# Optimization experiments

Measured on AMD Instinct MI355X. Metric: run time of the kernel, lower is better.

Reference implementation:

```python
import jax, jax.numpy as jnp
import numpy as np

D_MODEL = 2048
N_HEADS = 16
N_KV = 4
GROUP = N_HEADS // N_KV  # 4
D_K = D_MODEL // N_HEADS  # 128
D_V = D_MODEL // N_KV     # 512
THETA = 10000.0
Q_DIM = N_HEADS * D_K
K_DIM = N_KV * D_K
V_DIM = N_KV * D_V


def _apply_rope(t, sin, cos):
    # t: [B, H, L, D]; sin/cos: [L, D] broadcast over batch/heads
    half = t.shape[-1] // 2
    x1, x2 = t[..., :half], t[..., half:]
    rot = jnp.concatenate([-x2, x1], axis=-1)
    return t * cos + rot * sin


def setup_inputs() -> dict:
    key = jax.random.key(0)
    k1, k2, k3 = jax.random.split(key, 3)
    x = jax.random.normal(k1, (2, 2048, D_MODEL), dtype=jnp.float32)
    # attn_proj: Linear(d_model -> Q_DIM+K_DIM+V_DIM, bias=False); stored as [in, out]
    W_attn = jax.random.normal(k2, (D_MODEL, Q_DIM + K_DIM + V_DIM), dtype=jnp.float32) * 0.02
    # out_proj: Linear(n_heads*d_v -> d_model) with bias
    W_out = jax.random.normal(k3, (N_HEADS * D_V, D_MODEL), dtype=jnp.float32) * 0.02
    b_out = jnp.zeros((D_MODEL,), dtype=jnp.float32)
    return {"x": x, "W_attn": W_attn, "W_out": W_out, "b_out": b_out}


def reference(x, W_attn, W_out, b_out):
    B, L, _ = x.shape
    qkv = x @ W_attn  # [B, L, Q_DIM+K_DIM+V_DIM]
    q = qkv[..., :Q_DIM].reshape(B, L, N_HEADS, D_K).transpose(0, 2, 1, 3)          # [B,H,L,dk]
    k = qkv[..., Q_DIM:Q_DIM + K_DIM].reshape(B, L, N_KV, D_K).transpose(0, 2, 1, 3)  # [B,Hkv,L,dk]
    v = qkv[..., Q_DIM + K_DIM:].reshape(B, L, N_KV, D_V).transpose(0, 2, 1, 3)       # [B,Hkv,L,dv]

    # RoPE (computed in float32, as in source)
    inv_freq = 1.0 / (THETA ** (jnp.arange(0, D_K, 2, dtype=jnp.float32) / D_K))
    freqs = jnp.arange(L, dtype=jnp.float32)[:, None] * inv_freq[None, :]  # [L, dk/2]
    ang = jnp.concatenate([freqs, freqs], axis=-1)                          # [L, dk]
    sin, cos = jnp.sin(ang), jnp.cos(ang)
    q = _apply_rope(q.astype(jnp.float32), sin, cos).astype(x.dtype)
    k = _apply_rope(k.astype(jnp.float32), sin, cos).astype(x.dtype)

    # GQA: repeat_interleave(group, dim=1) is equivalent to grouping q heads as [kv, group]
    qg = q.reshape(B, N_KV, GROUP, L, D_K)
    scores = jnp.einsum('bkgqd,bkld->bkgql', qg, k) / (D_K ** 0.5)  # [B,Hkv,G,L,L]
    probs = jax.nn.softmax(scores, axis=-1)
    ctx = jnp.einsum('bkgql,bkle->bkgqe', probs, v)  # [B,Hkv,G,L,dv]
    ctx = ctx.reshape(B, N_HEADS, L, D_V).transpose(0, 2, 1, 3).reshape(B, L, N_HEADS * D_V)
    return ctx @ W_out + b_out
```

## Files before the change

kernel.cpp:

```cpp
#include <hip/hip_runtime.h>

typedef unsigned short u16;
typedef float f32x4 __attribute__((ext_vector_type(4)));
typedef __bf16 bf16x8 __attribute__((ext_vector_type(8)));

#define DEV static __device__ __forceinline__

DEV u16 f2bf(float f) {
  union { float f; unsigned u; } c; c.f = f;
  unsigned u = c.u;
  u += 0x7fffu + ((u >> 16) & 1u);
  return (u16)(u >> 16);
}
DEV float bf2f(u16 h) {
  union { float f; unsigned u; } c; c.u = ((unsigned)h) << 16;
  return c.f;
}
DEV f32x4 MFMA(bf16x8 a, bf16x8 b, f32x4 c) {
  return __builtin_amdgcn_mfma_f32_16x16x32_bf16(a, b, c, 0, 0, 0);
}
DEV unsigned cvt_pk_bf16(float a, float b) {
  unsigned r;
  asm("v_cvt_pk_bf16_f32 %0, %1, %2" : "=v"(r) : "v"(a), "v"(b));
  return r;
}
DEV float ex2(float x) { return __builtin_amdgcn_exp2f(x); }
DEV void glds16(const void* src, void* lds) {
  __builtin_amdgcn_global_load_lds(
      (__attribute__((address_space(1))) void*)src,
      (__attribute__((address_space(3))) void*)lds, 16, 0, 0);
}
DEV void barrier_raw() {
  __builtin_amdgcn_sched_barrier(0);
  asm volatile("s_barrier" ::: "memory");
  __builtin_amdgcn_sched_barrier(0);
}
#define VMCNT(N)                                              \
  do {                                                        \
    asm volatile("s_waitcnt vmcnt(" #N ")" ::: "memory");     \
    __builtin_amdgcn_sched_barrier(0);                        \
  } while (0)


__global__ void prep_kernel(const float* __restrict__ x, const float* __restrict__ W_attn,
                            float* __restrict__ sinT, float* __restrict__ cosT,
                            u16* __restrict__ xb, u16* __restrict__ WbT) {
  __shared__ u16 tile[64][72];
  const int bk = blockIdx.x, t = threadIdx.x;
  if (bk < 512) {
    int idx = bk * 256 + t;
    int l = idx >> 6, i = idx & 63;
    float inv = __expf(-((float)(2 * i) / 128.0f) * 9.210340371976184f);
    float ang = (float)l * inv;
    sinT[idx] = sinf(ang);
    cosT[idx] = cosf(ang);
  } else if (bk < 8704) {
    int i = ((bk - 512) * 256 + t) * 4;
    float4 v = *(const float4*)(x + i);
    ushort4 o;
    o.x = f2bf(v.x); o.y = f2bf(v.y); o.z = f2bf(v.z); o.w = f2bf(v.w);
    *(ushort4*)(xb + i) = o;
  } else {
    int idx = bk - 8704;
    int c0 = (idx % 72) * 64, r0 = (idx / 72) * 64;
    int tc = (t & 15) * 4, tr = t >> 4;
#pragma unroll
    for (int i = 0; i < 4; ++i) {
      int r = tr + i * 16;
      float4 v = *(const float4*)(W_attn + (size_t)(r0 + r) * 4608 + c0 + tc);
      tile[tc + 0][r] = f2bf(v.x);
      tile[tc + 1][r] = f2bf(v.y);
      tile[tc + 2][r] = f2bf(v.z);
      tile[tc + 3][r] = f2bf(v.w);
    }
    __syncthreads();
#pragma unroll
    for (int i = 0; i < 4; ++i) {
      int cc = tr + i * 16;
      ushort4 o;
      o.x = tile[cc][tc]; o.y = tile[cc][tc + 1];
      o.z = tile[cc][tc + 2]; o.w = tile[cc][tc + 3];
      *(ushort4*)(WbT + (size_t)(c0 + cc) * 2048 + r0 + tc) = o;
    }
  }
}

__global__ void transpose_cast64(const float* __restrict__ in, u16* __restrict__ out,
                                 int R, int C) {
  __shared__ u16 tile[64][72];
  int c0 = blockIdx.x * 64, r0 = blockIdx.y * 64;
  int t = threadIdx.x;
  int tc = (t & 15) * 4, tr = t >> 4;
#pragma unroll
  for (int i = 0; i < 4; ++i) {
    int r = tr + i * 16;
    float4 v = *(const float4*)(in + (size_t)(r0 + r) * C + c0 + tc);
    tile[tc + 0][r] = f2bf(v.x);
    tile[tc + 1][r] = f2bf(v.y);
    tile[tc + 2][r] = f2bf(v.z);
    tile[tc + 3][r] = f2bf(v.w);
  }
  __syncthreads();
#pragma unroll
  for (int i = 0; i < 4; ++i) {
    int cc = tr + i * 16;
    ushort4 o;
    o.x = tile[cc][tc]; o.y = tile[cc][tc + 1];
    o.z = tile[cc][tc + 2]; o.w = tile[cc][tc + 3];
    *(ushort4*)(out + (size_t)(c0 + cc) * R + r0 + tc) = o;
  }
}

__global__ __launch_bounds__(512) void gemm1_8ph(const u16* __restrict__ A,
                                                 const u16* __restrict__ Bt,
                                                 u16* __restrict__ C) {
  constexpr int K = 2048, N = 4608, NT = 32;
  __shared__ __align__(16) u16 lA[2][2][8192];
  __shared__ __align__(16) u16 lB[2][2][8192];
  const int t = threadIdx.x, w = t >> 6, l = t & 63;
  const int lr = l & 15, lg = l >> 4;
  const int wr = w >> 2, wn = w & 3;
  const int swz = (blockIdx.x & 7) * 36 + (blockIdx.x >> 3);
  const int bm = swz & 15, bn = swz >> 4;

  const size_t aBase = (size_t)(bm * 256) * K;
  const size_t bBase = (size_t)(bn * 256) * K;
  const int lslog = (t & 3) ^ ((t >> 3) & 3);
  const int r128 = t >> 2;
  const int aswz = (lg ^ ((lr >> 1) & 3)) << 4;

  auto stA = [&](int buf, int kk, int tile) {
#pragma unroll
    for (int i = 0; i < 2; ++i) {
      int row = i * 128 + r128;
      glds16(A + aBase + (size_t)row * K + tile * 64 + kk * 32 + lslog * 8,
             &lA[buf][kk][i * 4096 + t * 8]);
    }
  };
  auto stB = [&](int buf, int kk, int tile) {
#pragma unroll
    for (int i = 0; i < 2; ++i) {
      int row = i * 128 + r128;
      glds16(Bt + bBase + (size_t)row * K + tile * 64 + kk * 32 + lslog * 8,
             &lB[buf][kk][i * 4096 + t * 8]);
    }
  };

  f32x4 acc[8][4];
#pragma unroll
  for (int f = 0; f < 8; ++f)
#pragma unroll
    for (int g = 0; g < 4; ++g) acc[f][g] = f32x4{0.f, 0.f, 0.f, 0.f};

  stA(0, 0, 0); stB(0, 0, 0); stA(0, 1, 0); stB(0, 1, 0); stA(1, 0, 1); stB(1, 0, 1);
  VMCNT(8);
  barrier_raw();

  auto PH = [&](int buf, int kk, int mh, auto&& st) {
    bf16x8 af[4], bb[4];
    const char* pA = (const char*)lA[buf][kk];
    const char* pB = (const char*)lB[buf][kk];
#pragma unroll
    for (int f = 0; f < 4; ++f) {
      af[f] = *(const bf16x8*)(pA + (wr * 128 + (mh * 4 + f) * 16 + lr) * 64 + aswz);
      bb[f] = *(const bf16x8*)(pB + (wn * 64 + f * 16 + lr) * 64 + aswz);
    }
    st();
    __builtin_amdgcn_s_setprio(1);
#pragma unroll
    for (int f = 0; f < 4; ++f)
#pragma unroll
      for (int g = 0; g < 4; ++g)
        acc[mh * 4 + f][g] = MFMA(af[f], bb[g], acc[mh * 4 + f][g]);
    __builtin_amdgcn_s_setprio(0);
  };
  auto NOST = [] {};

  for (int i = 0; i < NT / 2 - 1; ++i) {
    const int t1 = 2 * i + 1, t2 = 2 * i + 2, t3 = 2 * i + 3;
    PH(0, 0, 0, [&] { stA(1, 1, t1); });            barrier_raw();
    PH(0, 0, 1, [&] { stB(1, 1, t1); }); VMCNT(8);  barrier_raw();
    PH(0, 1, 0, [&] { stA(0, 0, t2); });            barrier_raw();
    PH(0, 1, 1, [&] { stB(0, 0, t2); }); VMCNT(8);  barrier_raw();
    PH(1, 0, 0, [&] { stA(0, 1, t2); });            barrier_raw();
    PH(1, 0, 1, [&] { stB(0, 1, t2); }); VMCNT(8);  barrier_raw();
    PH(1, 1, 0, [&] { stA(1, 0, t3); });            barrier_raw();
    PH(1, 1, 1, [&] { stB(1, 0, t3); }); VMCNT(8);  barrier_raw();
  }
  PH(0, 0, 0, [&] { stA(1, 1, NT - 1); });           barrier_raw();
  PH(0, 0, 1, [&] { stB(1, 1, NT - 1); }); VMCNT(8); barrier_raw();
  PH(0, 1, 0, NOST);                                 barrier_raw();
  PH(0, 1, 1, NOST);                       VMCNT(4); barrier_raw();
  PH(1, 0, 0, NOST);                                 barrier_raw();
  PH(1, 0, 1, NOST);                       VMCNT(0); barrier_raw();
  PH(1, 1, 0, NOST);                                 barrier_raw();
  PH(1, 1, 1, NOST);

  const int crow0 = bm * 256 + wr * 128;
  const int ccol0 = bn * 256 + wn * 64;
#pragma unroll
  for (int f = 0; f < 8; ++f)
#pragma unroll
    for (int g = 0; g < 4; ++g)
#pragma unroll
      for (int j = 0; j < 4; ++j)
        C[(size_t)(crow0 + f * 16 + lg * 4 + j) * N + ccol0 + g * 16 + lr] =
            f2bf(acc[f][g][j]);
}

template <int WRITE_F32, int K, int N>
__global__ __launch_bounds__(512) void gemm_4ph(const u16* __restrict__ A,
                                                const u16* __restrict__ Bt,
                                                u16* __restrict__ Cb,
                                                float* __restrict__ Cf,
                                                const float* __restrict__ bias) {
  constexpr int NT = K / 64;
  constexpr int NBN = N / 128;
  __shared__ __align__(16) u16 lA[2][2][8192];
  __shared__ __align__(16) u16 lB[2][2][4096];
  const int t = threadIdx.x, w = t >> 6, l = t & 63;
  const int lr = l & 15, lg = l >> 4;
  const int wr = w >> 1, wn = w & 1;
  const int swz = (blockIdx.x & 7) * (2 * NBN) + (blockIdx.x >> 3);
  const int bm = swz & 15, bn = swz >> 4;

  const size_t aBase = (size_t)(bm * 256) * K;
  const size_t bBase = (size_t)(bn * 128) * K;
  const int lslog = (t & 3) ^ ((t >> 3) & 3);
  const int r128 = t >> 2;
  const int aswz = (lg ^ ((lr >> 1) & 3)) << 4;

  auto stA = [&](int buf, int kk, int tile) {
#pragma unroll
    for (int i = 0; i < 2; ++i) {
      int row = i * 128 + r128;
      glds16(A + aBase + (size_t)row * K + tile * 64 + kk * 32 + lslog * 8,
             &lA[buf][kk][i * 4096 + t * 8]);
    }
  };
  auto stB = [&](int buf, int kk, int tile) {
    glds16(Bt + bBase + (size_t)r128 * K + tile * 64 + kk * 32 + lslog * 8,
           &lB[buf][kk][t * 8]);
  };

  f32x4 acc[4][4];
#pragma unroll
  for (int f = 0; f < 4; ++f)
#pragma unroll
    for (int g = 0; g < 4; ++g) acc[f][g] = f32x4{0.f, 0.f, 0.f, 0.f};

  stA(0, 0, 0); stB(0, 0, 0); stA(0, 1, 0); stB(0, 1, 0); stA(1, 0, 1); stB(1, 0, 1);
  VMCNT(6);
  barrier_raw();

  auto PH = [&](int buf, int kk, auto&& st) {
    bf16x8 af[4], bb[4];
    const char* pA = (const char*)lA[buf][kk];
    const char* pB = (const char*)lB[buf][kk];
#pragma unroll
    for (int f = 0; f < 4; ++f) {
      af[f] = *(const bf16x8*)(pA + (wr * 64 + f * 16 + lr) * 64 + aswz);
      bb[f] = *(const bf16x8*)(pB + (wn * 64 + f * 16 + lr) * 64 + aswz);
    }
    st();
    __builtin_amdgcn_s_setprio(1);
#pragma unroll
    for (int f = 0; f < 4; ++f)
#pragma unroll
      for (int g = 0; g < 4; ++g)
        acc[f][g] = MFMA(af[f], bb[g], acc[f][g]);
    __builtin_amdgcn_s_setprio(0);
  };
  auto NOST = [] {};

  for (int i = 0; i < NT / 2 - 1; ++i) {
    const int t1 = 2 * i + 1, t2 = 2 * i + 2, t3 = 2 * i + 3;
    PH(0, 0, [&] { stA(1, 1, t1); stB(1, 1, t1); }); VMCNT(6); barrier_raw();
    PH(0, 1, [&] { stA(0, 0, t2); stB(0, 0, t2); }); VMCNT(6); barrier_raw();
    PH(1, 0, [&] { stA(0, 1, t2); stB(0, 1, t2); }); VMCNT(6); barrier_raw();
    PH(1, 1, [&] { stA(1, 0, t3); stB(1, 0, t3); }); VMCNT(6); barrier_raw();
  }
  PH(0, 0, [&] { stA(1, 1, NT - 1); stB(1, 1, NT - 1); }); VMCNT(6); barrier_raw();
  PH(0, 1, NOST);                                          VMCNT(3); barrier_raw();
  PH(1, 0, NOST);                                          VMCNT(0); barrier_raw();
  PH(1, 1, NOST);

  const int crow0 = bm * 256 + wr * 64;
  const int ccol0 = bn * 128 + wn * 64;
#pragma unroll
  for (int g = 0; g < 4; ++g) {
    float bv = WRITE_F32 ? bias[ccol0 + g * 16 + lr] : 0.f;
#pragma unroll
    for (int f = 0; f < 4; ++f)
#pragma unroll
      for (int j = 0; j < 4; ++j) {
        size_t off = (size_t)(crow0 + f * 16 + lg * 4 + j) * N + ccol0 + g * 16 + lr;
        if (WRITE_F32) Cf[off] = acc[f][g][j] + bv;
        else           Cb[off] = f2bf(acc[f][g][j]);
      }
  }
}

__global__ void ropevt_kernel(u16* __restrict__ qkv, const float* __restrict__ sinT,
                              const float* __restrict__ cosT, u16* __restrict__ vT) {
  __shared__ u16 tile[32][33];
  const int bk = blockIdx.x, t = threadIdx.x;
  if (bk < 20480) {
    int idx = bk * 256 + t;
    int d = idx & 63;
    int rh = idx >> 6;
    int head = rh % 20;
    int row = rh / 20;
    int lpos = row & 2047;
    int col = head < 16 ? head * 128 : 2048 + (head - 16) * 128;
    float sc = head < 16 ? 0.12751743561938476f : 1.0f;
    u16* p = qkv + (size_t)row * 4608 + col;
    float x1 = bf2f(p[d]), x2 = bf2f(p[d + 64]);
    float c = cosT[lpos * 64 + d], s = sinT[lpos * 64 + d];
    p[d]      = f2bf((x1 * c - x2 * s) * sc);
    p[d + 64] = f2bf((x2 * c + x1 * s) * sc);
  } else {
    int idx = bk - 20480;
    int bx = idx & 15, by = (idx >> 4) & 63, bkv = idx >> 10;
    int b = bkv >> 2, kv = bkv & 3;
    int e0 = bx * 32, l0 = by * 32;
    const u16* src = qkv + (size_t)(b * 2048) * 4608 + 2560 + kv * 512;
    int tx = t & 31, ty = t >> 5;
    for (int i = 0; i < 32; i += 8)
      tile[ty + i][tx] = src[(size_t)(l0 + ty + i) * 4608 + e0 + tx];
    __syncthreads();
    u16* dst = vT + (size_t)(bkv * 512) * 2048;
    int pi = ((tx >> 2) & 3) * 8 + ((tx >> 4) & 1) * 4 + (tx & 3);
    for (int i = 0; i < 32; i += 8)
      dst[(size_t)(e0 + ty + i) * 2048 + l0 + pi] = tile[tx][ty + i];
  }
}

__global__ __launch_bounds__(512, 2) void attn_kernel(
    const u16* __restrict__ qkv, const u16* __restrict__ vT,
    u16* __restrict__ ctxb) {
  const int wg = blockIdx.x;
  const int pg = wg & 7, qt = wg >> 3;
  const int kvg = pg & 3, b = pg >> 2;
  const int t = threadIdx.x, w = t >> 6, l = t & 63;
  const int lr = l & 15, lg = l >> 4;
  const int h4 = w >> 1, eh = w & 1;
  const int h = kvg * 4 + h4;

  __shared__ __align__(16) u16 lK[2][64 * 128];
  __shared__ __align__(16) u16 lV[2][512 * 64];

  f32x4 zero = {0.f, 0.f, 0.f, 0.f};

  bf16x8 qf[2][4];
  const size_t qbase = (size_t)(b * 2048 + qt * 32);
#pragma unroll
  for (int m = 0; m < 2; ++m)
#pragma unroll
    for (int dc = 0; dc < 4; ++dc)
      qf[m][dc] = *(const bf16x8*)(qkv + (qbase + m * 16 + lr) * 4608 + h * 128 + dc * 32 + lg * 8);

  f32x4 acc[2][16];
#pragma unroll
  for (int m = 0; m < 2; ++m)
#pragma unroll
    for (int e = 0; e < 16; ++e) acc[m][e] = zero;
  float m_r[2] = {-1e30f, -1e30f};
  float l_r[2] = {0.f, 0.f};

  const size_t kbase = (size_t)(b * 2048) * 4608 + 2048 + kvg * 128;
  const size_t vbase = (size_t)((b * 4 + kvg) * 512) * 2048;

  const int krow = t >> 4;
  const int kp = t & 15;
  const int ks = (kp & 8) | ((kp ^ (krow & 7)) & 7);
  const u16* ksrc0 = qkv + kbase + (size_t)krow * 4608 + ks * 8;
  const int vs = (t & 7) ^ ((t >> 3) & 7);
  const int ve0 = (t >> 3) * 2 + (vs >> 2);
  const u16* vsrc0 = vT + vbase + (size_t)ve0 * 2048 + (vs & 3) * 8;

  const int vfoff = (eh * 128 + (lr >> 1)) * 128 +
                    (((((lr & 1) << 2) | lg) ^ ((lr >> 1) & 7)) << 4);

  auto stage = [&](int bi, int kv0) {
#pragma unroll
    for (int i = 0; i < 2; ++i)
      glds16(ksrc0 + (size_t)(kv0 + i * 32) * 4608, &lK[bi][i * 4096 + t * 8]);
#pragma unroll
    for (int hh = 0; hh < 2; ++hh)
#pragma unroll
      for (int i = 0; i < 4; ++i)
        glds16(vsrc0 + (kv0 + hh * 32) + (size_t)i * 262144,
               &lV[bi][hh * 16384 + i * 4096 + t * 8]);
  };

  stage(0, 0);

  auto half_body = [&](const char* lKc, const char* lVc) {
    f32x4 sT[2][2];
    sT[0][0] = zero; sT[0][1] = zero; sT[1][0] = zero; sT[1][1] = zero;
    __builtin_amdgcn_s_setprio(1);
#pragma unroll
    for (int dc = 0; dc < 4; ++dc) {
      int slot = dc * 4 + lg;
      int sw = (slot & 8) | ((slot ^ (lr & 7)) & 7);
#pragma unroll
      for (int kt = 0; kt < 2; ++kt) {
        bf16x8 kf = *(const bf16x8*)(lKc + (kt * 16 + lr) * 256 + sw * 16);
        sT[kt][0] = MFMA(kf, qf[0][dc], sT[kt][0]);
        sT[kt][1] = MFMA(kf, qf[1][dc], sT[kt][1]);
      }
    }
    __builtin_amdgcn_s_setprio(0);

    float lmax[2];
#pragma unroll
    for (int m = 0; m < 2; ++m) {
      float a0 = fmaxf(fmaxf(sT[0][m][0], sT[0][m][1]), fmaxf(sT[0][m][2], sT[0][m][3]));
      float a1 = fmaxf(fmaxf(sT[1][m][0], sT[1][m][1]), fmaxf(sT[1][m][2], sT[1][m][3]));
      lmax[m] = fmaxf(a0, a1);
    }
    bool need = (lmax[0] > m_r[0] + 11.5f) || (lmax[1] > m_r[1] + 11.5f);
    if (__any(need)) {
#pragma unroll
      for (int m = 0; m < 2; ++m) {
        float r = lmax[m];
        r = fmaxf(r, __shfl_xor(r, 16));
        r = fmaxf(r, __shfl_xor(r, 32));
        float mn = fmaxf(m_r[m], r);
        float al = ex2(m_r[m] - mn);
        m_r[m] = mn; l_r[m] *= al;
        float alj[4];
#pragma unroll
        for (int j = 0; j < 4; ++j) alj[j] = __shfl(al, lg * 4 + j);
#pragma unroll
        for (int e = 0; e < 16; ++e)
#pragma unroll
          for (int j = 0; j < 4; ++j) acc[m][e][j] *= alj[j];
      }
    }

    bf16x8 pf[2];
#pragma unroll
    for (int m = 0; m < 2; ++m) {
      float p0 = ex2(sT[0][m][0] - m_r[m]), p1 = ex2(sT[0][m][1] - m_r[m]);
      float p2 = ex2(sT[0][m][2] - m_r[m]), p3 = ex2(sT[0][m][3] - m_r[m]);
      float p4 = ex2(sT[1][m][0] - m_r[m]), p5 = ex2(sT[1][m][1] - m_r[m]);
      float p6 = ex2(sT[1][m][2] - m_r[m]), p7 = ex2(sT[1][m][3] - m_r[m]);
      l_r[m] += ((p0 + p1) + (p2 + p3)) + ((p4 + p5) + (p6 + p7));
      union { bf16x8 v; unsigned wd[4]; } u;
      u.wd[0] = cvt_pk_bf16(p0, p1);
      u.wd[1] = cvt_pk_bf16(p2, p3);
      u.wd[2] = cvt_pk_bf16(p4, p5);
      u.wd[3] = cvt_pk_bf16(p6, p7);
      pf[m] = u.v;
    }

    __builtin_amdgcn_s_setprio(1);
#pragma unroll
    for (int e = 0; e < 16; ++e) {
      bf16x8 vf = *(const bf16x8*)(lVc + vfoff + e * 1024);
      acc[0][e] = MFMA(pf[0], vf, acc[0][e]);
      acc[1][e] = MFMA(pf[1], vf, acc[1][e]);
    }
    __builtin_amdgcn_s_setprio(0);
  };

  for (int it = 0; it < 32; ++it) {
    const int cur = it & 1;
    __syncthreads();
    if (it + 1 < 32) stage(cur ^ 1, 64 * (it + 1));
    const char* lKc = (const char*)lK[cur];
    const char* lVc = (const char*)lV[cur];
    half_body(lKc, lVc);
    half_body(lKc + 8192, lVc + 32768);
  }

#pragma unroll
  for (int m = 0; m < 2; ++m) {
    float s = l_r[m];
    s += __shfl_xor(s, 16);
    s += __shfl_xor(s, 32);
    l_r[m] = s;
  }
#pragma unroll
  for (int m = 0; m < 2; ++m) {
    float linv[4];
#pragma unroll
    for (int j = 0; j < 4; ++j) linv[j] = 1.0f / __shfl(l_r[m], lg * 4 + j);
    const size_t orow0 = qbase + m * 16 + lg * 4;
#pragma unroll
    for (int e = 0; e < 16; ++e)
#pragma unroll
      for (int j = 0; j < 4; ++j)
        ctxb[(orow0 + j) * 8192 + h * 512 + eh * 256 + e * 16 + lr] =
            f2bf(acc[m][e][j] * linv[j]);
  }
}

extern "C" void kernel_launch(void* const* d_in, const int* in_sizes, int n_in,
                              void* d_out, int out_size, void* d_ws, size_t ws_size,
                              hipStream_t stream) {
  const float* x      = (const float*)d_in[0];
  const float* W_attn = (const float*)d_in[1];
  const float* W_out  = (const float*)d_in[2];
  const float* b_out  = (const float*)d_in[3];
  float* out = (float*)d_out;
  char* ws = (char*)d_ws;

  if (ws_size < 158334976u) return;

  float* sinT = (float*)(ws + 0);
  float* cosT = (float*)(ws + 524288);
  u16* xb   = (u16*)(ws + 1048576);
  u16* WbT  = (u16*)(ws + 17825792);
  u16* qkvb = (u16*)(ws + 36700160);
  u16* vT   = (u16*)(ws + 74448896);
  u16* ctxb = (u16*)(ws + 91226112);
  u16* WobT = (u16*)(ws + 1048576);

  prep_kernel<<<11008, 256, 0, stream>>>(x, W_attn, sinT, cosT, xb, WbT);
  gemm1_8ph<<<288, 512, 0, stream>>>(xb, WbT, qkvb);
  ropevt_kernel<<<28672, 256, 0, stream>>>(qkvb, sinT, cosT, vT);
  attn_kernel<<<512, 512, 0, stream>>>(qkvb, vT, ctxb);
  transpose_cast64<<<dim3(32, 128), 256, 0, stream>>>(W_out, WobT, 8192, 2048);
  gemm_4ph<1, 8192, 2048><<<256, 512, 0, stream>>>(ctxb, WobT, nullptr, out, b_out);
}
```

Before: 555.2 us.

## Use 256x256-tile split-K GEMM for output projection with partial-sum add

The output projection now reuses the 8-phase 256x256-tile GEMM instead of the 256x128 4-phase kernel. K is split in two so the grid stays at 256 blocks. The first K-half writes the result plus bias, the second writes an fp32 partial into a dead workspace region, and a new elementwise kernel adds the two. The larger tiles raise operand reuse per block. The cost is an extra kernel launch and a full fp32 read-modify-write of the output plus the partial buffer.

```diff
diff --git a/kernel.cpp b/kernel.cpp
--- a/kernel.cpp
+++ b/kernel.cpp
@@ -111,20 +111,32 @@
   }
 }
 
-__global__ __launch_bounds__(512) void gemm1_8ph(const u16* __restrict__ A,
-                                                 const u16* __restrict__ Bt,
-                                                 u16* __restrict__ C) {
-  constexpr int K = 2048, N = 4608, NT = 32;
+template <int MODE>
+__global__ __launch_bounds__(512) void gemm_8ph(const u16* __restrict__ A,
+                                                const u16* __restrict__ Bt,
+                                                u16* __restrict__ Cb,
+                                                float* __restrict__ Cf,
+                                                float* __restrict__ P1,
+                                                const float* __restrict__ bias) {
+  constexpr int KF = MODE == 0 ? 2048 : 8192;
+  constexpr int NT = MODE == 0 ? 32 : 64;
+  constexpr int N  = MODE == 0 ? 4608 : 2048;
   __shared__ __align__(16) u16 lA[2][2][8192];
   __shared__ __align__(16) u16 lB[2][2][8192];
   const int t = threadIdx.x, w = t >> 6, l = t & 63;
   const int lr = l & 15, lg = l >> 4;
   const int wr = w >> 2, wn = w & 3;
-  const int swz = (blockIdx.x & 7) * 36 + (blockIdx.x >> 3);
-  const int bm = swz & 15, bn = swz >> 4;
-
-  const size_t aBase = (size_t)(bm * 256) * K;
-  const size_t bBase = (size_t)(bn * 256) * K;
+  int bm, bn, ks;
+  if (MODE == 0) {
+    const int swz = (blockIdx.x & 7) * 36 + (blockIdx.x >> 3);
+    bm = swz & 15; bn = swz >> 4; ks = 0;
+  } else {
+    const int swz = (blockIdx.x & 7) * 32 + (blockIdx.x >> 3);
+    bm = swz & 15; bn = (swz >> 4) & 7; ks = swz >> 7;
+  }
+
+  const size_t aBase = (size_t)(bm * 256) * KF + ks * 4096;
+  const size_t bBase = (size_t)(bn * 256) * KF + ks * 4096;
   const int lslog = (t & 3) ^ ((t >> 3) & 3);
   const int r128 = t >> 2;
   const int aswz = (lg ^ ((lr >> 1) & 3)) << 4;
@@ -133,7 +145,7 @@
 #pragma unroll
     for (int i = 0; i < 2; ++i) {
       int row = i * 128 + r128;
-      glds16(A + aBase + (size_t)row * K + tile * 64 + kk * 32 + lslog * 8,
+      glds16(A + aBase + (size_t)row * KF + tile * 64 + kk * 32 + lslog * 8,
              &lA[buf][kk][i * 4096 + t * 8]);
     }
   };
@@ -141,7 +153,7 @@
 #pragma unroll
     for (int i = 0; i < 2; ++i) {
       int row = i * 128 + r128;
-      glds16(Bt + bBase + (size_t)row * K + tile * 64 + kk * 32 + lslog * 8,
+      glds16(Bt + bBase + (size_t)row * KF + tile * 64 + kk * 32 + lslog * 8,
              &lB[buf][kk][i * 4096 + t * 8]);
     }
   };
@@ -198,107 +210,44 @@
 
   const int crow0 = bm * 256 + wr * 128;
   const int ccol0 = bn * 256 + wn * 64;
-#pragma unroll
-  for (int f = 0; f < 8; ++f)
-#pragma unroll
-    for (int g = 0; g < 4; ++g)
-#pragma unroll
-      for (int j = 0; j < 4; ++j)
-        C[(size_t)(crow0 + f * 16 + lg * 4 + j) * N + ccol0 + g * 16 + lr] =
-            f2bf(acc[f][g][j]);
-}
-
-template <int WRITE_F32, int K, int N>
-__global__ __launch_bounds__(512) void gemm_4ph(const u16* __restrict__ A,
-                                                const u16* __restrict__ Bt,
-                                                u16* __restrict__ Cb,
-                                                float* __restrict__ Cf,
-                                                const float* __restrict__ bias) {
-  constexpr int NT = K / 64;
-  constexpr int NBN = N / 128;
-  __shared__ __align__(16) u16 lA[2][2][8192];
-  __shared__ __align__(16) u16 lB[2][2][4096];
-  const int t = threadIdx.x, w = t >> 6, l = t & 63;
-  const int lr = l & 15, lg = l >> 4;
-  const int wr = w >> 1, wn = w & 1;
-  const int swz = (blockIdx.x & 7) * (2 * NBN) + (blockIdx.x >> 3);
-  const int bm = swz & 15, bn = swz >> 4;
-
-  const size_t aBase = (size_t)(bm * 256) * K;
-  const size_t bBase = (size_t)(bn * 128) * K;
-  const int lslog = (t & 3) ^ ((t >> 3) & 3);
-  const int r128 = t >> 2;
-  const int aswz = (lg ^ ((lr >> 1) & 3)) << 4;
-
-  auto stA = [&](int buf, int kk, int tile) {
-#pragma unroll
-    for (int i = 0; i < 2; ++i) {
-      int row = i * 128 + r128;
-      glds16(A + aBase + (size_t)row * K + tile * 64 + kk * 32 + lslog * 8,
-             &lA[buf][kk][i * 4096 + t * 8]);
-    }
-  };
-  auto stB = [&](int buf, int kk, int tile) {
-    glds16(Bt + bBase + (size_t)r128 * K + tile * 64 + kk * 32 + lslog * 8,
-           &lB[buf][kk][t * 8]);
-  };
-
-  f32x4 acc[4][4];
-#pragma unroll
-  for (int f = 0; f < 4; ++f)
-#pragma unroll
-    for (int g = 0; g < 4; ++g) acc[f][g] = f32x4{0.f, 0.f, 0.f, 0.f};
-
-  stA(0, 0, 0); stB(0, 0, 0); stA(0, 1, 0); stB(0, 1, 0); stA(1, 0, 1); stB(1, 0, 1);
-  VMCNT(6);
-  barrier_raw();
-
-  auto PH = [&](int buf, int kk, auto&& st) {
-    bf16x8 af[4], bb[4];
-    const char* pA = (const char*)lA[buf][kk];
-    const char* pB = (const char*)lB[buf][kk];
-#pragma unroll
-    for (int f = 0; f < 4; ++f) {
-      af[f] = *(const bf16x8*)(pA + (wr * 64 + f * 16 + lr) * 64 + aswz);
-      bb[f] = *(const bf16x8*)(pB + (wn * 64 + f * 16 + lr) * 64 + aswz);
-    }
-    st();
-    __builtin_amdgcn_s_setprio(1);
-#pragma unroll
-    for (int f = 0; f < 4; ++f)
+  if (MODE == 0) {
+#pragma unroll
+    for (int f = 0; f < 8; ++f)
 #pragma unroll
       for (int g = 0; g < 4; ++g)
-        acc[f][g] = MFMA(af[f], bb[g], acc[f][g]);
-    __builtin_amdgcn_s_setprio(0);
-  };
-  auto NOST = [] {};
-
-  for (int i = 0; i < NT / 2 - 1; ++i) {
-    const int t1 = 2 * i + 1, t2 = 2 * i + 2, t3 = 2 * i + 3;
-    PH(0, 0, [&] { stA(1, 1, t1); stB(1, 1, t1); }); VMCNT(6); barrier_raw();
-    PH(0, 1, [&] { stA(0, 0, t2); stB(0, 0, t2); }); VMCNT(6); barrier_raw();
-    PH(1, 0, [&] { stA(0, 1, t2); stB(0, 1, t2); }); VMCNT(6); barrier_raw();
-    PH(1, 1, [&] { stA(1, 0, t3); stB(1, 0, t3); }); VMCNT(6); barrier_raw();
-  }
-  PH(0, 0, [&] { stA(1, 1, NT - 1); stB(1, 1, NT - 1); }); VMCNT(6); barrier_raw();
-  PH(0, 1, NOST);                                          VMCNT(3); barrier_raw();
-  PH(1, 0, NOST);                                          VMCNT(0); barrier_raw();
-  PH(1, 1, NOST);
-
-  const int crow0 = bm * 256 + wr * 64;
-  const int ccol0 = bn * 128 + wn * 64;
-#pragma unroll
-  for (int g = 0; g < 4; ++g) {
-    float bv = WRITE_F32 ? bias[ccol0 + g * 16 + lr] : 0.f;
-#pragma unroll
-    for (int f = 0; f < 4; ++f)
-#pragma unroll
-      for (int j = 0; j < 4; ++j) {
-        size_t off = (size_t)(crow0 + f * 16 + lg * 4 + j) * N + ccol0 + g * 16 + lr;
-        if (WRITE_F32) Cf[off] = acc[f][g][j] + bv;
-        else           Cb[off] = f2bf(acc[f][g][j]);
-      }
-  }
+#pragma unroll
+        for (int j = 0; j < 4; ++j)
+          Cb[(size_t)(crow0 + f * 16 + lg * 4 + j) * N + ccol0 + g * 16 + lr] =
+              f2bf(acc[f][g][j]);
+  } else if (ks == 0) {
+#pragma unroll
+    for (int g = 0; g < 4; ++g) {
+      float bv = bias[ccol0 + g * 16 + lr];
+#pragma unroll
+      for (int f = 0; f < 8; ++f)
+#pragma unroll
+        for (int j = 0; j < 4; ++j)
+          Cf[(size_t)(crow0 + f * 16 + lg * 4 + j) * N + ccol0 + g * 16 + lr] =
+              acc[f][g][j] + bv;
+    }
+  } else {
+#pragma unroll
+    for (int f = 0; f < 8; ++f)
+#pragma unroll
+      for (int g = 0; g < 4; ++g)
+#pragma unroll
+        for (int j = 0; j < 4; ++j)
+          P1[(size_t)(crow0 + f * 16 + lg * 4 + j) * N + ccol0 + g * 16 + lr] =
+              acc[f][g][j];
+  }
+}
+
+__global__ void addp_kernel(float* __restrict__ out, const float* __restrict__ P1) {
+  int i = (blockIdx.x * 256 + threadIdx.x) * 4;
+  float4 a = *(const float4*)(out + i);
+  float4 b = *(const float4*)(P1 + i);
+  a.x += b.x; a.y += b.y; a.z += b.z; a.w += b.w;
+  *(float4*)(out + i) = a;
 }
 
 __global__ void ropevt_kernel(u16* __restrict__ qkv, const float* __restrict__ sinT,
@@ -518,11 +467,13 @@
   u16* vT   = (u16*)(ws + 74448896);
   u16* ctxb = (u16*)(ws + 91226112);
   u16* WobT = (u16*)(ws + 1048576);
+  float* P1 = (float*)(ws + 36700160);
 
   prep_kernel<<<11008, 256, 0, stream>>>(x, W_attn, sinT, cosT, xb, WbT);
-  gemm1_8ph<<<288, 512, 0, stream>>>(xb, WbT, qkvb);
+  gemm_8ph<0><<<288, 512, 0, stream>>>(xb, WbT, qkvb, nullptr, nullptr, nullptr);
   ropevt_kernel<<<28672, 256, 0, stream>>>(qkvb, sinT, cosT, vT);
   attn_kernel<<<512, 512, 0, stream>>>(qkvb, vT, ctxb);
   transpose_cast64<<<dim3(32, 128), 256, 0, stream>>>(W_out, WobT, 8192, 2048);
-  gemm_4ph<1, 8192, 2048><<<256, 512, 0, stream>>>(ctxb, WobT, nullptr, out, b_out);
-}
+  gemm_8ph<1><<<256, 512, 0, stream>>>(ctxb, WobT, nullptr, out, P1, b_out);
+  addp_kernel<<<8192, 256, 0, stream>>>(out, P1);
+}
```

Measured after the change: 558.1 us. No clear change (+0.5%).
